# Kernel tuning notes

Measured on AMD Instinct MI355X. Metric: run time of the kernel, lower is better.

Reference implementation:

```python
import jax, jax.numpy as jnp
import numpy as np

N_OP, N_TAB, N_COL, N_PRED = 131072, 32768, 131072, 65536
NCF = 32
H = 512
NUM_GRAPHS = 64
EPS = 1e-5  # torch LayerNorm default
# fixed relation order: (src_type, dst_type)
RELS = [('table', 'operator'), ('predicate', 'operator'), ('column', 'operator'),
        ('column', 'predicate'), ('operator', 'operator'), ('table', 'table'), ('column', 'column')]
NNODE = {'operator': N_OP, 'table': N_TAB, 'column': N_COL, 'predicate': N_PRED}
EDGES = [262144, 262144, 262144, 262144, 262144, 32768, 131072]


def setup_inputs() -> dict:
    key = jax.random.key(0)
    ks = iter(jax.random.split(key, 80))
    def nrm(shape, fan_in):
        return jax.random.normal(next(ks), shape, jnp.float32) / np.sqrt(fan_in).astype(np.float32)
    inp = {
        'x_operator': jax.random.normal(next(ks), (N_OP, 4), jnp.float32),
        'x_table': jax.random.normal(next(ks), (N_TAB, 2), jnp.float32),
        'x_column': jax.random.normal(next(ks), (N_COL, NCF), jnp.float32),
        'x_predicate': jax.random.normal(next(ks), (N_PRED, 4), jnp.float32),
        'W_op': nrm((4, H), 4), 'b_op': jnp.zeros((H,), jnp.float32),
        'W_tab': nrm((2, H), 2), 'b_tab': jnp.zeros((H,), jnp.float32),
        'W_col': nrm((NCF, H), NCF), 'b_col': jnp.zeros((H,), jnp.float32),
        'W_pred': nrm((4, H), 4), 'b_pred': jnp.zeros((H,), jnp.float32),
        'conv1_Wl': nrm((7, H, H), H), 'conv1_bl': jnp.zeros((7, H), jnp.float32),
        'conv1_Wr': nrm((7, H, H), H),
        'conv2_Wl': nrm((7, H, H), H), 'conv2_bl': jnp.zeros((7, H), jnp.float32),
        'conv2_Wr': nrm((7, H, H), H),
        'g1': jnp.ones((H,), jnp.float32), 'beta1': jnp.zeros((H,), jnp.float32),
        'g2': jnp.ones((H,), jnp.float32), 'beta2': jnp.zeros((H,), jnp.float32),
        'W_out': nrm((H, 1), H), 'b_out': jnp.zeros((1,), jnp.float32),
    }
    for i, (s, d) in enumerate(RELS):
        e = EDGES[i]
        inp[f'src{i}'] = jax.random.randint(next(ks), (e,), 0, NNODE[s], jnp.int32)
        inp[f'dst{i}'] = jax.random.randint(next(ks), (e,), 0, NNODE[d], jnp.int32)
    inp['batch_operator'] = jnp.sort(jax.random.randint(next(ks), (N_OP,), 0, NUM_GRAPHS, jnp.int32))
    return inp


def _layer_norm(x, g, b):
    m = jnp.mean(x, -1, keepdims=True)
    v = jnp.mean((x - m) ** 2, -1, keepdims=True)
    return (x - m) * jax.lax.rsqrt(v + EPS) * g + b


def _segment_mean(vals, idx, n):
    s = jax.ops.segment_sum(vals, idx, num_segments=n)
    c = jax.ops.segment_sum(jnp.ones(idx.shape, vals.dtype), idx, num_segments=n)
    return s / jnp.maximum(c, 1.0)[:, None]


def _sage(x_src, x_dst, src, dst, Wl, bl, Wr, n_dst):
    # PyG SAGEConv: lin_l(mean of neighbor msgs) + lin_r(root), lin_r has no bias
    agg = _segment_mean(x_src[src], dst, n_dst)
    return agg @ Wl + bl + x_dst @ Wr


def _forward(x_operator, x_table, x_column, x_predicate,
             W_op, b_op, W_tab, b_tab, W_col, b_col, W_pred, b_pred,
             conv1_Wl, conv1_bl, conv1_Wr, conv2_Wl, conv2_bl, conv2_Wr,
             g1, beta1, g2, beta2, W_out, b_out, edges, batch_operator):
    h = {'operator': x_operator @ W_op + b_op,
         'table': x_table @ W_tab + b_tab,
         'column': x_column @ W_col + b_col,
         'predicate': x_predicate @ W_pred + b_pred}

    def hetero(h, Wl, bl, Wr):
        outs = {}
        for i, (s, d) in enumerate(RELS):
            src, dst = edges[i]
            o = _sage(h[s], h[d], src, dst, Wl[i], bl[i], Wr[i], NNODE[d])
            outs.setdefault(d, []).append(o)
        # HeteroConv aggr='mean' across relations sharing a dst node type
        return {k: sum(v) / len(v) for k, v in outs.items()}

    h = hetero(h, conv1_Wl, conv1_bl, conv1_Wr)
    h = {k: _layer_norm(jax.nn.elu(v), g1, beta1) for k, v in h.items()}  # dropout = eval identity
    h = hetero(h, conv2_Wl, conv2_bl, conv2_Wr)
    h = {k: _layer_norm(jax.nn.elu(v), g2, beta2) for k, v in h.items()}
    pooled = _segment_mean(h['operator'], batch_operator, NUM_GRAPHS)  # global_mean_pool
    return (pooled @ W_out + b_out).squeeze()


def reference(x_operator, x_table, x_column, x_predicate,
              W_op, b_op, W_tab, b_tab, W_col, b_col, W_pred, b_pred,
              conv1_Wl, conv1_bl, conv1_Wr, conv2_Wl, conv2_bl, conv2_Wr,
              g1, beta1, g2, beta2, W_out, b_out,
              src0, dst0, src1, dst1, src2, dst2, src3, dst3,
              src4, dst4, src5, dst5, src6, dst6, batch_operator):
    edges = [(src0, dst0), (src1, dst1), (src2, dst2), (src3, dst3),
             (src4, dst4), (src5, dst5), (src6, dst6)]
    return _forward(x_operator, x_table, x_column, x_predicate,
                    W_op, b_op, W_tab, b_tab, W_col, b_col, W_pred, b_pred,
                    conv1_Wl, conv1_bl, conv1_Wr, conv2_Wl, conv2_bl, conv2_Wr,
                    g1, beta1, g2, beta2, W_out, b_out, edges, batch_operator)
```

## Files before the change

kernel.cpp:

```cpp
#include <hip/hip_runtime.h>
#include <hip/hip_bf16.h>

typedef unsigned short u16;
typedef __attribute__((ext_vector_type(8))) short bf16x8;
typedef __attribute__((ext_vector_type(4))) short bf16x4;
typedef __attribute__((ext_vector_type(4))) float f32x4;

typedef __attribute__((address_space(1))) const void gv_t;
typedef __attribute__((address_space(3))) void lv_t;

#define DEVINL __device__ __forceinline__

DEVINL float bf2f(u16 s) { union { unsigned u; float f; } v; v.u = ((unsigned)s) << 16; return v.f; }
DEVINL u16 f2bf(float f) {
  union { float f; unsigned u; } v; v.f = f;
  return (u16)((v.u + 0x7FFFu + ((v.u >> 16) & 1u)) >> 16);
}

__global__ void probe_k(float* __restrict__ out, float v) { out[threadIdx.x] = v; }

struct PackPtrs { const float* wl2; const float* wr2; u16* bt[5]; };
__global__ __launch_bounds__(256) void pack_multi(PackPtrs p) {
  int j = blockIdx.x >> 10;
  int idx = (blockIdx.x & 1023) * 256 + threadIdx.x;
  int k = idx >> 9, n = idx & 511;
  float v;
  if (j < 4) {
    int r = (j == 3) ? 4 : j;
    v = p.wl2[((size_t)r * 512 + k) * 512 + n];
  } else {
    size_t o = (size_t)k * 512 + n;
    v = p.wr2[o] + p.wr2[o + 262144] + p.wr2[o + 524288] + p.wr2[o + 1048576];
  }
  p.bt[j][(size_t)n * 512 + k] = f2bf(v * 0.25f);
}

struct FoldPtrs { const float* a[8]; const float* w[2]; u16* bt[4]; };
__constant__ int   c_off[19] = {0,16,24,56,64,320,328,360,368,400,416,424,440,696,704,960,1216,1224,1256};
__constant__ int   c_ai[18]  = {0,1,2,3,4,5,6,7,6, 0,1,0, 4,5,4, 4,5,2};
__constant__ int   c_wi[18]  = {0,0,0,0,0,0,0,0,1, 0,0,1, 0,0,1, 0,0,1};
__constant__ int   c_r0[18]  = {0,0,1,1,2,2,4,4,0, 5,5,5, 6,6,6, 3,3,3};
__constant__ float c_sc[18]  = {0.25f,0.25f,0.25f,0.25f,0.25f,0.25f,0.25f,0.25f,0.25f,
                                1.f,1.f,1.f, 1.f,1.f,1.f, 1.f,1.f,1.f};
__constant__ int   c_bt[18]  = {0,0,0,0,0,0,0,0,0, 1,1,1, 2,2,2, 3,3,3};
__constant__ int   c_K[18]   = {64,64,64,64,64,64,64,64,64, 64,64,64, 128,128,128, 64,64,64};
__constant__ int   c_ko[18]  = {0,2,3,7,8,40,41,45,46, 0,2,3, 0,32,33, 0,32,33};

__global__ __launch_bounds__(256) void fold_multi(FoldPtrs p) {
  __shared__ float red[256];
  int b = blockIdx.x;
  int j = 0;
#pragma unroll
  for (int t = 1; t < 18; ++t) j += (b >= c_off[t]);
  int rel = b - c_off[j];
  int f = rel >> 3, nb = rel & 7;
  int tid = threadIdx.x;
  int n = nb * 64 + (tid & 63);
  int kg = tid >> 6;
  const float* A = p.a[c_ai[j]] + (size_t)f * 512;
  const float* W = p.w[c_wi[j]];
  int k0 = kg * 128;
  float acc = 0.f;
  if (j != 8) {
    const float* Wp = W + (size_t)c_r0[j] * 512 * 512 + n;
#pragma unroll 16
    for (int k = k0; k < k0 + 128; ++k) acc += A[k] * Wp[(size_t)k * 512];
  } else {
    const float* W0 = W + n;
    const float* W1 = W + (size_t)262144 + n;
    const float* W2 = W + (size_t)524288 + n;
    const float* W4 = W + (size_t)1048576 + n;
#pragma unroll 8
    for (int k = k0; k < k0 + 128; ++k) {
      size_t o = (size_t)k * 512;
      acc += A[k] * (W0[o] + W1[o] + W2[o] + W4[o]);
    }
  }
  red[tid] = acc;
  __syncthreads();
  if (kg == 0) {
    float v = red[tid] + red[tid + 64] + red[tid + 128] + red[tid + 192];
    p.bt[c_bt[j]][(size_t)n * c_K[j] + c_ko[j] + f] = f2bf(v * c_sc[j]);
  }
}

struct VFPtrs { const float* bl[5]; const float* bvec[5]; const float* w; float* out[5]; };
__constant__ int   c_vi[5][4] = {{0,1,2,4},{0,1,2,4},{5,-1,-1,-1},{6,-1,-1,-1},{3,-1,-1,-1}};
__constant__ float c_vs[5]    = {0.25f,0.25f,1.f,1.f,1.f};

__global__ __launch_bounds__(256) void vecfold_multi(VFPtrs p) {
  __shared__ float red[256];
  int j = blockIdx.x >> 4, blk = blockIdx.x & 15;
  int tid = threadIdx.x;
  int n = blk * 32 + (tid & 31);
  int kg = tid >> 5;
  const float* bv = p.bvec[j];
  float a = 0.f;
  if (bv) {
    int i1 = c_vi[j][1];
    const float* W0 = p.w + (size_t)c_vi[j][0] * 262144 + n;
    if (i1 < 0) {
#pragma unroll 16
      for (int k = kg * 64; k < kg * 64 + 64; ++k) a += bv[k] * W0[(size_t)k * 512];
    } else {
      const float* W1 = p.w + (size_t)c_vi[j][1] * 262144 + n;
      const float* W2 = p.w + (size_t)c_vi[j][2] * 262144 + n;
      const float* W3 = p.w + (size_t)c_vi[j][3] * 262144 + n;
#pragma unroll 8
      for (int k = kg * 64; k < kg * 64 + 64; ++k) {
        size_t o = (size_t)k * 512;
        a += bv[k] * (W0[o] + W1[o] + W2[o] + W3[o]);
      }
    }
  }
  red[tid] = a;
  __syncthreads();
  if (kg == 0) {
    float v = 0.f;
#pragma unroll
    for (int q = 0; q < 8; ++q) v += red[(tid & 31) + q * 32];
    float bsum = p.bl[j][c_vi[j][0] * 512 + n];
    if (c_vi[j][1] >= 0) {
      bsum += p.bl[j][c_vi[j][1] * 512 + n];
      bsum += p.bl[j][c_vi[j][2] * 512 + n];
      bsum += p.bl[j][c_vi[j][3] * 512 + n];
    }
    p.out[j][n] = (v + bsum) * c_vs[j];
  }
}

struct EdgePtrs { const int* dst[7]; const int* src[7]; };
__constant__ int c_hoff[8]  = {0,1024,2048,3072,4096,5120,5248,5760};
__constant__ int c_hbase[7] = {0,131072,262144,393216,458752,589824,622592};
__constant__ int c_hne[7]   = {262144,262144,262144,262144,262144,32768,131072};

__global__ __launch_bounds__(256) void hist_multi(EdgePtrs p, int* __restrict__ cnt) {
  int b = blockIdx.x;
  int j = 0;
#pragma unroll
  for (int t = 1; t < 7; ++t) j += (b >= c_hoff[t]);
  int i = (b - c_hoff[j]) * 256 + threadIdx.x;
  if (i < c_hne[j]) atomicAdd(&cnt[c_hbase[j] + p.dst[j][i]], 1);
}

__global__ __launch_bounds__(256) void fill_multi(EdgePtrs p, int* __restrict__ cursor,
                                                  int* __restrict__ esrc) {
  int b = blockIdx.x;
  int j = 0;
#pragma unroll
  for (int t = 1; t < 7; ++t) j += (b >= c_hoff[t]);
  int i = (b - c_hoff[j]) * 256 + threadIdx.x;
  if (i < c_hne[j]) {
    int pos = atomicAdd(&cursor[c_hbase[j] + p.dst[j][i]], 1);
    esrc[pos] = p.src[j][i];
  }
}

__global__ void scan1_k(const int* __restrict__ in, int* __restrict__ out,
                        int* __restrict__ part, int n) {
  __shared__ int s[256];
  int t = threadIdx.x;
  int base = blockIdx.x * 1024 + t * 4;
  int x0 = 0, x1 = 0, x2 = 0, x3 = 0;
  if (base < n) x0 = in[base];
  if (base + 1 < n) x1 = in[base + 1];
  if (base + 2 < n) x2 = in[base + 2];
  if (base + 3 < n) x3 = in[base + 3];
  int tsum = x0 + x1 + x2 + x3;
  s[t] = tsum;
  __syncthreads();
  for (int off = 1; off < 256; off <<= 1) {
    int v = (t >= off) ? s[t - off] : 0;
    __syncthreads();
    s[t] += v;
    __syncthreads();
  }
  int excl = s[t] - tsum;
  if (base < n) out[base] = excl;
  if (base + 1 < n) out[base + 1] = excl + x0;
  if (base + 2 < n) out[base + 2] = excl + x0 + x1;
  if (base + 3 < n) out[base + 3] = excl + x0 + x1 + x2;
  if (t == 255) part[blockIdx.x] = s[255];
}

__global__ void scan2_k(int* __restrict__ part, int nb) {
  __shared__ int s[1024];
  int t = threadIdx.x;
  int orig = (t < nb) ? part[t] : 0;
  s[t] = orig;
  __syncthreads();
  for (int off = 1; off < 1024; off <<= 1) {
    int v = (t >= off) ? s[t - off] : 0;
    __syncthreads();
    s[t] += v;
    __syncthreads();
  }
  if (t < nb) part[t] = s[t] - orig;
}

__global__ void scan3_k(int* __restrict__ out, int* __restrict__ cursor,
                        const int* __restrict__ part, int n) {
  int i = blockIdx.x * 256 + threadIdx.x;
  if (i < n) {
    int v = out[i] + part[i >> 10];
    out[i] = v;
    cursor[i] = v;
  }
}

__global__ void raw_agg(const int* __restrict__ offs, const int* __restrict__ esrc,
                        const float* __restrict__ x, int F, u16* __restrict__ A1,
                        int K, int colOff, int indCol, int nd) {
  int row = blockIdx.x * 32 + (threadIdx.x >> 3);
  if (row >= nd) return;
  int j = threadIdx.x & 7;
  int e0 = offs[row], e1 = offs[row + 1];
  float acc[4] = {0.f, 0.f, 0.f, 0.f};
  for (int e = e0; e < e1; ++e) {
    int s = esrc[e];
#pragma unroll
    for (int u = 0; u < 4; ++u) {
      int f = j + u * 8;
      if (f < F) acc[u] += x[(size_t)s * F + f];
    }
  }
  float inv = (e1 > e0) ? 1.f / (float)(e1 - e0) : 0.f;
#pragma unroll
  for (int u = 0; u < 4; ++u) {
    int f = j + u * 8;
    if (f < F) A1[(size_t)row * K + colOff + f] = f2bf(acc[u] * inv);
  }
  if (j == 0) A1[(size_t)row * K + indCol] = f2bf((e1 > e0) ? 1.f : 0.f);
}

struct RawPtrs { const int* offs; const int* esrc; const float* x[4]; u16* A1; };
__constant__ int c_gF[4]    = {2,4,32,4};
__constant__ int c_gco[4]   = {0,3,8,41};
__constant__ int c_gic[4]   = {2,7,40,45};
__constant__ int c_gcsrb[4] = {0,131072,262144,458752};

__global__ __launch_bounds__(256) void raw_multi(RawPtrs p, int s0) {
  int j = blockIdx.x >> 10;
  int row = (blockIdx.x & 1023) * 32 + (threadIdx.x >> 3);
  int jj = threadIdx.x & 7;
  const int* offs = p.offs + c_gcsrb[j] + s0;
  const float* x = p.x[j];
  int F = c_gF[j];
  int e0 = offs[row], e1 = offs[row + 1];
  float acc[4] = {0.f, 0.f, 0.f, 0.f};
  for (int e = e0; e < e1; ++e) {
    int s = p.esrc[e];
#pragma unroll
    for (int u = 0; u < 4; ++u) {
      int f = jj + u * 8;
      if (f < F) acc[u] += x[(size_t)s * F + f];
    }
  }
  float inv = (e1 > e0) ? 1.f / (float)(e1 - e0) : 0.f;
#pragma unroll
  for (int u = 0; u < 4; ++u) {
    int f = jj + u * 8;
    if (f < F) p.A1[(size_t)row * 64 + c_gco[j] + f] = f2bf(acc[u] * inv);
  }
  if (jj == 0) p.A1[(size_t)row * 64 + c_gic[j]] = f2bf((e1 > e0) ? 1.f : 0.f);
}

__global__ void a1_root(const float* __restrict__ x, int rowBase, u16* __restrict__ A1,
                        int K, int rootOff, int nd, int lf) {
  int idx = blockIdx.x * 256 + threadIdx.x;
  int i = idx >> lf, f = idx & ((1 << lf) - 1);
  if (i >= nd) return;
  A1[(size_t)i * K + rootOff + f] = f2bf(x[(((size_t)(rowBase + i)) << lf) + f]);
}

template <bool FIRST>
__global__ __launch_bounds__(256) void gather_acc(
    const int* __restrict__ offs, const int* __restrict__ esrc,
    const u16* __restrict__ hT, const float* __restrict__ bias,
    u16* __restrict__ acc, int s0, int s1) {
  int w = blockIdx.x * 4 + (threadIdx.x >> 6);
  int l = threadIdx.x & 63;
  int e0 = offs[w], e1 = offs[w + 1];
  float sum[8] = {0.f, 0.f, 0.f, 0.f, 0.f, 0.f, 0.f, 0.f};
  bool found = false;
  for (int e = e0; e < e1; ++e) {
    int s = esrc[e];
    if (s >= s0 && s < s1) {
      found = true;
      bf16x8 v = *(const bf16x8*)&hT[(size_t)(s - s0) * 512 + l * 8];
#pragma unroll
      for (int j = 0; j < 8; ++j) sum[j] += bf2f((u16)v[j]);
    }
  }
  float inv = (e1 > e0) ? 1.f / (float)(e1 - e0) : 0.f;
  u16* ap = acc + (size_t)w * 512 + l * 8;
  bf16x8 r;
  if (FIRST) {
#pragma unroll
    for (int j = 0; j < 8; ++j) r[j] = (short)f2bf(bias[l * 8 + j] + sum[j] * inv);
    *(bf16x8*)ap = r;
  } else {
    if (!found) return;
    bf16x8 old = *(const bf16x8*)ap;
#pragma unroll
    for (int j = 0; j < 8; ++j) r[j] = (short)f2bf(bf2f((u16)old[j]) + sum[j] * inv);
    *(bf16x8*)ap = r;
  }
}

template <bool ELU, bool ACC, int K>
__global__ __launch_bounds__(256) void gemm_k(
    const u16* __restrict__ A, const u16* __restrict__ BT,
    const float* __restrict__ bias, u16* __restrict__ C, int M) {
  __shared__ u16 As[128 * 64];
  __shared__ u16 Bs[128 * 64];
  int tid = threadIdx.x;
  int wid = tid >> 6, lane = tid & 63;
  int wm = wid >> 1, wn = wid & 1;
  int bm = blockIdx.x * 128, bn = blockIdx.y * 128;
  int r16 = lane & 15, hi4 = lane >> 4;
  int srow = tid >> 3;
  int scol = ((tid & 7) ^ (srow & 7)) * 8;
  int sw = r16 & 7;
  f32x4 acc[4][4];
#pragma unroll
  for (int i = 0; i < 4; ++i)
#pragma unroll
    for (int j = 0; j < 4; ++j) acc[i][j] = (f32x4){0.f, 0.f, 0.f, 0.f};

#pragma unroll
  for (int k0 = 0; k0 < K; k0 += 64) {
    __syncthreads();
#pragma unroll
    for (int i = 0; i < 4; ++i) {
      const u16* ga = A + (size_t)(bm + i * 32 + srow) * K + k0 + scol;
      const u16* gb = BT + (size_t)(bn + i * 32 + srow) * K + k0 + scol;
      __builtin_amdgcn_global_load_lds((gv_t*)ga, (lv_t*)(As + i * 2048 + wid * 512), 16, 0, 0);
      __builtin_amdgcn_global_load_lds((gv_t*)gb, (lv_t*)(Bs + i * 2048 + wid * 512), 16, 0, 0);
    }
    __syncthreads();
#pragma unroll
    for (int kk = 0; kk < 64; kk += 32) {
      bf16x8 af[4], bfr[4];
#pragma unroll
      for (int f = 0; f < 4; ++f) {
        int grp = (kk >> 3) + hi4;
        af[f]  = *(const bf16x8*)&As[(wm * 64 + f * 16 + r16) * 64 + ((grp ^ sw) << 3)];
        bfr[f] = *(const bf16x8*)&Bs[(wn * 64 + f * 16 + r16) * 64 + ((grp ^ sw) << 3)];
      }
#pragma unroll
      for (int mf = 0; mf < 4; ++mf)
#pragma unroll
        for (int nf = 0; nf < 4; ++nf)
          acc[mf][nf] = __builtin_amdgcn_mfma_f32_16x16x32_bf16(bfr[nf], af[mf], acc[mf][nf], 0, 0, 0);
    }
  }
#pragma unroll
  for (int mf = 0; mf < 4; ++mf) {
    int r = bm + wm * 64 + mf * 16 + r16;
#pragma unroll
    for (int nf = 0; nf < 4; ++nf) {
      int c0 = bn + wn * 64 + nf * 16 + hi4 * 4;
      u16* cp = C + (size_t)r * 512 + c0;
      bf16x4 oldv;
      if (ACC) oldv = *(const bf16x4*)cp;
      f32x4 bv;
      if (bias) bv = *(const f32x4*)&bias[c0];
      bf16x4 res;
#pragma unroll
      for (int j = 0; j < 4; ++j) {
        float v = acc[mf][nf][j] + (bias ? bv[j] : 0.f);
        if (ACC) v += bf2f((u16)oldv[j]);
        if (ELU) v = v > 0.f ? v : expm1f(v);
        res[j] = (short)f2bf(v);
      }
      *(bf16x4*)cp = res;
    }
  }
}

template <bool ACC>
__global__ __launch_bounds__(256) void gemm_t(
    const u16* __restrict__ A, const u16* __restrict__ BT, u16* __restrict__ C) {
  __shared__ u16 As[128 * 64];
  __shared__ u16 Bs[128 * 64];
  int b = blockIdx.x;
  int u = (b & 7) * 128 + (b >> 3);
  int bm = (u >> 2) * 128;
  int bn = (u & 3) * 128;
  int tid = threadIdx.x;
  int wid = tid >> 6, lane = tid & 63;
  int wm = wid >> 1, wn = wid & 1;
  int r16 = lane & 15, hi4 = lane >> 4;
  int srow = tid >> 3;
  int scol = ((tid & 7) ^ (srow & 7)) * 8;
  int sw = r16 & 7;
  f32x4 acc[4][4];
#pragma unroll
  for (int i = 0; i < 4; ++i)
#pragma unroll
    for (int j = 0; j < 4; ++j) acc[i][j] = (f32x4){0.f, 0.f, 0.f, 0.f};

#pragma unroll
  for (int k0 = 0; k0 < 512; k0 += 64) {
    __syncthreads();
#pragma unroll
    for (int i = 0; i < 4; ++i) {
      const u16* ga = A + (size_t)(bm + i * 32 + srow) * 512 + k0 + scol;
      const u16* gb = BT + (size_t)(bn + i * 32 + srow) * 512 + k0 + scol;
      __builtin_amdgcn_global_load_lds((gv_t*)ga, (lv_t*)(As + i * 2048 + wid * 512), 16, 0, 0);
      __builtin_amdgcn_global_load_lds((gv_t*)gb, (lv_t*)(Bs + i * 2048 + wid * 512), 16, 0, 0);
    }
    __syncthreads();
#pragma unroll
    for (int kk = 0; kk < 64; kk += 32) {
      bf16x8 af[4], bfr[4];
#pragma unroll
      for (int f = 0; f < 4; ++f) {
        int grp = (kk >> 3) + hi4;
        af[f]  = *(const bf16x8*)&As[(wm * 64 + f * 16 + r16) * 64 + ((grp ^ sw) << 3)];
        bfr[f] = *(const bf16x8*)&Bs[(wn * 64 + f * 16 + r16) * 64 + ((grp ^ sw) << 3)];
      }
#pragma unroll
      for (int mf = 0; mf < 4; ++mf)
#pragma unroll
        for (int nf = 0; nf < 4; ++nf)
          acc[mf][nf] = __builtin_amdgcn_mfma_f32_16x16x32_bf16(bfr[nf], af[mf], acc[mf][nf], 0, 0, 0);
    }
  }
#pragma unroll
  for (int mf = 0; mf < 4; ++mf) {
    int r = bm + wm * 64 + mf * 16 + r16;
#pragma unroll
    for (int nf = 0; nf < 4; ++nf) {
      int c0 = bn + wn * 64 + nf * 16 + hi4 * 4;
      u16* cp = C + (size_t)r * 512 + c0;
      bf16x4 res;
      if (ACC) {
        bf16x4 oldv = *(const bf16x4*)cp;
#pragma unroll
        for (int j = 0; j < 4; ++j) res[j] = (short)f2bf(acc[mf][nf][j] + bf2f((u16)oldv[j]));
      } else {
#pragma unroll
        for (int j = 0; j < 4; ++j) res[j] = (short)f2bf(acc[mf][nf][j]);
      }
      *(bf16x4*)cp = res;
    }
  }
}

__global__ void ln_rows(u16* __restrict__ H, const float* __restrict__ g,
                        const float* __restrict__ be, int rows) {
  int w = blockIdx.x * 4 + (threadIdx.x >> 6);
  if (w >= rows) return;
  int l = threadIdx.x & 63;
  u16* p = H + (size_t)w * 512 + l * 8;
  bf16x8 v = *(const bf16x8*)p;
  float x[8];
  float s = 0.f;
#pragma unroll
  for (int j = 0; j < 8; ++j) { x[j] = bf2f((u16)v[j]); s += x[j]; }
#pragma unroll
  for (int m = 1; m < 64; m <<= 1) s += __shfl_xor(s, m, 64);
  float mean = s * (1.f / 512.f);
  float q = 0.f;
#pragma unroll
  for (int j = 0; j < 8; ++j) { float d = x[j] - mean; q += d * d; }
#pragma unroll
  for (int m = 1; m < 64; m <<= 1) q += __shfl_xor(q, m, 64);
  float rsd = rsqrtf(q * (1.f / 512.f) + 1e-5f);
  bf16x8 r;
#pragma unroll
  for (int j = 0; j < 8; ++j) {
    int c = l * 8 + j;
    r[j] = (short)f2bf((x[j] - mean) * rsd * g[c] + be[c]);
  }
  *(bf16x8*)p = r;
}

DEVINL int lowb(const int* a, int n, int v) {
  int lo = 0, hi = n;
  while (lo < hi) { int m = (lo + hi) >> 1; if (a[m] < v) lo = m + 1; else hi = m; }
  return lo;
}

__global__ __launch_bounds__(256) void pool1v(const u16* __restrict__ H,
                                              const int* __restrict__ batch, int nOp,
                                              const float* __restrict__ g2,
                                              const float* __restrict__ be2,
                                              float* __restrict__ pooled,
                                              int* __restrict__ cnts) {
  __shared__ float red[4][512];
  int gr = blockIdx.x >> 4, part = blockIdx.x & 15;
  int lo = lowb(batch, nOp, gr), hi = lowb(batch, nOp, gr + 1);
  if (part == 0 && threadIdx.x == 0) cnts[gr] = hi - lo;
  int len = hi - lo;
  int chunk = (len + 15) >> 4;
  int r0 = lo + part * chunk;
  int r1 = r0 + chunk;
  if (r1 > hi) r1 = hi;
  int wv = threadIdx.x >> 6, l = threadIdx.x & 63;
  float a[8] = {0.f, 0.f, 0.f, 0.f, 0.f, 0.f, 0.f, 0.f};
  float gv[8], bv[8];
#pragma unroll
  for (int j = 0; j < 8; ++j) { gv[j] = g2[l * 8 + j]; bv[j] = be2[l * 8 + j]; }
  for (int r = r0 + wv; r < r1; r += 4) {
    bf16x8 v = *(const bf16x8*)&H[(size_t)r * 512 + l * 8];
    float x[8];
    float s = 0.f;
#pragma unroll
    for (int j = 0; j < 8; ++j) {
      x[j] = bf2f((u16)v[j]);
      x[j] = x[j] > 0.f ? x[j] : expm1f(x[j]);
      s += x[j];
    }
#pragma unroll
    for (int m = 1; m < 64; m <<= 1) s += __shfl_xor(s, m, 64);
    float mean = s * (1.f / 512.f);
    float q = 0.f;
#pragma unroll
    for (int j = 0; j < 8; ++j) { float d = x[j] - mean; q += d * d; }
#pragma unroll
    for (int m = 1; m < 64; m <<= 1) q += __shfl_xor(q, m, 64);
    float rsd = rsqrtf(q * (1.f / 512.f) + 1e-5f);
#pragma unroll
    for (int j = 0; j < 8; ++j) a[j] += (x[j] - mean) * rsd * gv[j] + bv[j];
  }
#pragma unroll
  for (int j = 0; j < 8; ++j) red[wv][l * 8 + j] = a[j];
  __syncthreads();
  if (wv == 0) {
#pragma unroll
    for (int j = 0; j < 8; ++j) {
      int c = l * 8 + j;
      float s = red[0][c] + red[1][c] + red[2][c] + red[3][c];
      atomicAdd(&pooled[gr * 512 + c], s);
    }
  }
}

__global__ void pool2(const float* __restrict__ pooled, const int* __restrict__ cnts,
                      const float* __restrict__ Wout, const float* __restrict__ bout,
                      float* __restrict__ out) {
  int gg = blockIdx.x;
  int l = threadIdx.x;
  float s = 0.f;
#pragma unroll
  for (int j = 0; j < 8; ++j) {
    int c = l * 8 + j;
    s += pooled[gg * 512 + c] * Wout[c];
  }
#pragma unroll
  for (int m = 1; m < 64; m <<= 1) s += __shfl_xor(s, m, 64);
  if (l == 0) {
    int c = cnts[gg];
    if (c < 1) c = 1;
    out[gg] = s / (float)c + bout[0];
  }
}

extern "C" void kernel_launch(void* const* d_in, const int* in_sizes, int n_in,
                              void* d_out, int out_size, void* d_ws, size_t ws_size,
                              hipStream_t stream) {
  (void)in_sizes; (void)n_in; (void)out_size;
  const float* x_op   = (const float*)d_in[0];
  const float* x_tab  = (const float*)d_in[1];
  const float* x_col  = (const float*)d_in[2];
  const float* x_pred = (const float*)d_in[3];
  const float* W_op = (const float*)d_in[4],  *b_op = (const float*)d_in[5];
  const float* W_tab = (const float*)d_in[6], *b_tab = (const float*)d_in[7];
  const float* W_col = (const float*)d_in[8], *b_col = (const float*)d_in[9];
  const float* W_pred = (const float*)d_in[10], *b_pred = (const float*)d_in[11];
  const float* Wl1 = (const float*)d_in[12];
  const float* bl1 = (const float*)d_in[13];
  const float* Wr1 = (const float*)d_in[14];
  const float* Wl2 = (const float*)d_in[15];
  const float* bl2 = (const float*)d_in[16];
  const float* Wr2 = (const float*)d_in[17];
  const float* g1  = (const float*)d_in[18];
  const float* be1 = (const float*)d_in[19];
  const float* g2  = (const float*)d_in[20];
  const float* be2 = (const float*)d_in[21];
  const float* Wout = (const float*)d_in[22];
  const float* bout = (const float*)d_in[23];
  const int* SRC[7], *DST[7];
  for (int r = 0; r < 7; ++r) { SRC[r] = (const int*)d_in[24 + 2 * r]; DST[r] = (const int*)d_in[25 + 2 * r]; }
  const int* batch = (const int*)d_in[38];
  float* out = (float*)d_out;

  const int CSRB[7] = {0, 131072, 262144, 393216, 458752, 589824, 622592};
  const int TOT = 753664;
  const int NOP = 131072;

  char* ws = (char*)d_ws;
  u16* acc     = (u16*)ws;
  u16* h1      = (u16*)(ws + 134217728ull);
  int* curFul  = (int*)(ws + 134217728ull);
  u16* hT      = (u16*)(ws + 167772160ull);
  u16* A1      = (u16*)(ws + 234881024ull);
  int* offsFul = (int*)(ws + 243269632ull);
  int* esrcFul = (int*)(ws + 246284544ull);
  u16* BT2_0   = (u16*)(ws + 252182784ull);
  u16* BT2_1   = BT2_0 + 262144;
  u16* BT2_2   = BT2_1 + 262144;
  u16* BT2_4   = BT2_2 + 262144;
  u16* BT2rt   = BT2_4 + 262144;
  u16* BT1op   = (u16*)(ws + 254804224ull);
  u16* BT1tab  = (u16*)(ws + 254869760ull);
  u16* BT1col  = (u16*)(ws + 254935296ull);
  u16* BT1pr   = (u16*)(ws + 255066368ull);
  float* b1op  = (float*)(ws + 255131904ull);
  float* b1tab = b1op + 512, *b1col = b1op + 1024, *b1pr = b1op + 1536, *b2vec = b1op + 2048;
  float* pooled = (float*)(ws + 255142144ull);
  int* cnts     = (int*)(ws + 255273216ull);
  int* part     = (int*)(ws + 255273472ull);
  const size_t WS_NEED = 255277568ull;
  if (ws_size < WS_NEED) { probe_k<<<1, 64, 0, stream>>>(out, (float)ws_size); return; }

  (void)hipMemsetAsync(curFul, 0, 3014912ull, stream);
  EdgePtrs ep;
  for (int r = 0; r < 7; ++r) { ep.dst[r] = DST[r]; ep.src[r] = SRC[r]; }
  hist_multi<<<5760, 256, 0, stream>>>(ep, curFul);
  scan1_k<<<737, 256, 0, stream>>>(curFul, offsFul, part, TOT + 1);
  scan2_k<<<1, 1024, 0, stream>>>(part, 737);
  scan3_k<<<2945, 256, 0, stream>>>(offsFul, curFul, part, TOT + 1);
  fill_multi<<<5760, 256, 0, stream>>>(ep, curFul, esrcFul);

  PackPtrs pp;
  pp.wl2 = Wl2; pp.wr2 = Wr2;
  pp.bt[0] = BT2_0; pp.bt[1] = BT2_1; pp.bt[2] = BT2_2; pp.bt[3] = BT2_4; pp.bt[4] = BT2rt;
  pack_multi<<<5120, 256, 0, stream>>>(pp);
  (void)hipMemsetAsync(BT1op, 0, 65536 + 65536 + 131072 + 65536, stream);
  FoldPtrs fp;
  fp.a[0] = W_tab; fp.a[1] = b_tab; fp.a[2] = W_pred; fp.a[3] = b_pred;
  fp.a[4] = W_col; fp.a[5] = b_col; fp.a[6] = W_op;   fp.a[7] = b_op;
  fp.w[0] = Wl1;   fp.w[1] = Wr1;
  fp.bt[0] = BT1op; fp.bt[1] = BT1tab; fp.bt[2] = BT1col; fp.bt[3] = BT1pr;
  fold_multi<<<1256, 256, 0, stream>>>(fp);
  VFPtrs vp;
  vp.bl[0] = bl2; vp.bl[1] = bl1; vp.bl[2] = bl1; vp.bl[3] = bl1; vp.bl[4] = bl1;
  vp.bvec[0] = nullptr; vp.bvec[1] = b_op; vp.bvec[2] = b_tab; vp.bvec[3] = b_col; vp.bvec[4] = b_pred;
  vp.w = Wr1;
  vp.out[0] = b2vec; vp.out[1] = b1op; vp.out[2] = b1tab; vp.out[3] = b1col; vp.out[4] = b1pr;
  vecfold_multi<<<80, 256, 0, stream>>>(vp);

  (void)hipMemsetAsync(A1, 0, 32768ull * 64 * 2, stream);
  raw_agg<<<1024, 256, 0, stream>>>(offsFul + CSRB[5], esrcFul, x_tab, 2, A1, 64, 0, 2, 32768);
  a1_root<<<256, 256, 0, stream>>>(x_tab, 0, A1, 64, 3, 32768, 1);
  gemm_k<true, false, 64><<<dim3(256, 4), 256, 0, stream>>>(A1, BT1tab, b1tab, h1, 32768);
  ln_rows<<<8192, 256, 0, stream>>>(h1, g1, be1, 32768);
  gemm_t<false><<<1024, 256, 0, stream>>>(h1, BT2_0, hT);
  gather_acc<true><<<32768, 256, 0, stream>>>(offsFul + CSRB[0], esrcFul, hT, b2vec, acc, 0, 32768);

  (void)hipMemsetAsync(A1, 0, 32768ull * 64 * 2, stream);
  for (int q = 0; q < 2; ++q) {
    int qs = q * 32768;
    raw_agg<<<1024, 256, 0, stream>>>(offsFul + CSRB[3] + qs, esrcFul, x_col, 32, A1, 64, 0, 32, 32768);
    a1_root<<<512, 256, 0, stream>>>(x_pred, qs, A1, 64, 33, 32768, 2);
    gemm_k<true, false, 64><<<dim3(256, 4), 256, 0, stream>>>(A1, BT1pr, b1pr, h1, 32768);
    ln_rows<<<8192, 256, 0, stream>>>(h1, g1, be1, 32768);
    gemm_t<false><<<1024, 256, 0, stream>>>(h1, BT2_1, hT + (size_t)qs * 512);
  }
  gather_acc<false><<<32768, 256, 0, stream>>>(offsFul + CSRB[1], esrcFul, hT, nullptr, acc, 0, 65536);

  (void)hipMemsetAsync(A1, 0, 32768ull * 128 * 2, stream);
  for (int hs = 0; hs < 2; ++hs) {
    int S0 = hs * 65536;
    for (int q = 0; q < 2; ++q) {
      int qs = S0 + q * 32768;
      raw_agg<<<1024, 256, 0, stream>>>(offsFul + CSRB[6] + qs, esrcFul, x_col, 32, A1, 128, 0, 32, 32768);
      a1_root<<<4096, 256, 0, stream>>>(x_col, qs, A1, 128, 33, 32768, 5);
      gemm_k<true, false, 128><<<dim3(256, 4), 256, 0, stream>>>(A1, BT1col, b1col, h1, 32768);
      ln_rows<<<8192, 256, 0, stream>>>(h1, g1, be1, 32768);
      gemm_t<false><<<1024, 256, 0, stream>>>(h1, BT2_2, hT + (size_t)q * 32768 * 512);
    }
    gather_acc<false><<<32768, 256, 0, stream>>>(offsFul + CSRB[2], esrcFul, hT, nullptr,
                                                 acc, S0, S0 + 65536);
  }

  (void)hipMemsetAsync(A1, 0, 32768ull * 64 * 2, stream);
  for (int hs = 0; hs < 2; ++hs) {
    int S0 = hs * 65536;
    for (int q = 0; q < 2; ++q) {
      int qs = S0 + q * 32768;
      RawPtrs rp;
      rp.offs = offsFul; rp.esrc = esrcFul; rp.A1 = A1;
      rp.x[0] = x_tab; rp.x[1] = x_pred; rp.x[2] = x_col; rp.x[3] = x_op;
      raw_multi<<<4096, 256, 0, stream>>>(rp, qs);
      a1_root<<<512, 256, 0, stream>>>(x_op, qs, A1, 64, 46, 32768, 2);
      gemm_k<true, false, 64><<<dim3(256, 4), 256, 0, stream>>>(A1, BT1op, b1op, h1, 32768);
      ln_rows<<<8192, 256, 0, stream>>>(h1, g1, be1, 32768);
      gemm_t<true><<<1024, 256, 0, stream>>>(h1, BT2rt, acc + (size_t)qs * 512);
      gemm_t<false><<<1024, 256, 0, stream>>>(h1, BT2_4, hT + (size_t)q * 32768 * 512);
    }
    gather_acc<false><<<32768, 256, 0, stream>>>(offsFul + CSRB[4], esrcFul, hT, nullptr,
                                                 acc, S0, S0 + 65536);
  }

  (void)hipMemsetAsync(pooled, 0, 64 * 512 * 4, stream);
  pool1v<<<1024, 256, 0, stream>>>(acc, batch, NOP, g2, be2, pooled, cnts);
  pool2<<<64, 64, 0, stream>>>(pooled, cnts, Wout, bout, out);
}
```

Before: 1.619 ms.

## Fold layer-1 LayerNorm into second GEMM epilogue via row stats and column sums

Replaces the in-place LayerNorm pass over h1 with a stats-only kernel that writes a per-row mean and rstd. The gamma scale is folded into the packed conv2 weights, and precomputed column sums of gamma*W and beta*W let the gemm_t epilogue apply the normalization algebraically. This removes the LN write-back of the 32768x512 activation buffer, leaving only a read. gemm_k also switches to the swizzled 1D block ordering. The change adds a small precompute kernel, and the GEMM now runs on un-normalized bf16 inputs, which may shift rounding error.

```diff
diff --git a/kernel.cpp b/kernel.cpp
--- a/kernel.cpp
+++ b/kernel.cpp
@@ -19,7 +19,7 @@
 
 __global__ void probe_k(float* __restrict__ out, float v) { out[threadIdx.x] = v; }
 
-struct PackPtrs { const float* wl2; const float* wr2; u16* bt[5]; };
+struct PackPtrs { const float* wl2; const float* wr2; const float* g1; u16* bt[5]; };
 __global__ __launch_bounds__(256) void pack_multi(PackPtrs p) {
   int j = blockIdx.x >> 10;
   int idx = (blockIdx.x & 1023) * 256 + threadIdx.x;
@@ -32,7 +32,44 @@
     size_t o = (size_t)k * 512 + n;
     v = p.wr2[o] + p.wr2[o + 262144] + p.wr2[o + 524288] + p.wr2[o + 1048576];
   }
-  p.bt[j][(size_t)n * 512 + k] = f2bf(v * 0.25f);
+  p.bt[j][(size_t)n * 512 + k] = f2bf(v * 0.25f * p.g1[k]);
+}
+
+__global__ __launch_bounds__(256) void csbb_k(const float* __restrict__ wl2,
+                                              const float* __restrict__ wr2,
+                                              const float* __restrict__ g1,
+                                              const float* __restrict__ be1,
+                                              float* __restrict__ cs, float* __restrict__ bb) {
+  __shared__ float redA[256], redB[256];
+  int j = blockIdx.x >> 4;
+  int n = (blockIdx.x & 15) * 32 + (threadIdx.x & 31);
+  int kg = threadIdx.x >> 5;
+  float a = 0.f, b = 0.f;
+  for (int k = kg * 64; k < kg * 64 + 64; ++k) {
+    float w;
+    if (j < 4) {
+      int r = (j == 3) ? 4 : j;
+      w = wl2[((size_t)r * 512 + k) * 512 + n];
+    } else {
+      size_t o = (size_t)k * 512 + n;
+      w = wr2[o] + wr2[o + 262144] + wr2[o + 524288] + wr2[o + 1048576];
+    }
+    a += g1[k] * w;
+    b += be1[k] * w;
+  }
+  redA[threadIdx.x] = a;
+  redB[threadIdx.x] = b;
+  __syncthreads();
+  if (kg == 0) {
+    float va = 0.f, vb = 0.f;
+#pragma unroll
+    for (int q = 0; q < 8; ++q) {
+      va += redA[(threadIdx.x & 31) + q * 32];
+      vb += redB[(threadIdx.x & 31) + q * 32];
+    }
+    cs[j * 512 + n] = va * 0.25f;
+    bb[j * 512 + n] = vb * 0.25f;
+  }
 }
 
 struct FoldPtrs { const float* a[8]; const float* w[2]; u16* bt[4]; };
@@ -308,80 +345,10 @@
   }
 }
 
-template <bool ELU, bool ACC, int K>
+template <bool ELU, int K>
 __global__ __launch_bounds__(256) void gemm_k(
     const u16* __restrict__ A, const u16* __restrict__ BT,
-    const float* __restrict__ bias, u16* __restrict__ C, int M) {
-  __shared__ u16 As[128 * 64];
-  __shared__ u16 Bs[128 * 64];
-  int tid = threadIdx.x;
-  int wid = tid >> 6, lane = tid & 63;
-  int wm = wid >> 1, wn = wid & 1;
-  int bm = blockIdx.x * 128, bn = blockIdx.y * 128;
-  int r16 = lane & 15, hi4 = lane >> 4;
-  int srow = tid >> 3;
-  int scol = ((tid & 7) ^ (srow & 7)) * 8;
-  int sw = r16 & 7;
-  f32x4 acc[4][4];
-#pragma unroll
-  for (int i = 0; i < 4; ++i)
-#pragma unroll
-    for (int j = 0; j < 4; ++j) acc[i][j] = (f32x4){0.f, 0.f, 0.f, 0.f};
-
-#pragma unroll
-  for (int k0 = 0; k0 < K; k0 += 64) {
-    __syncthreads();
-#pragma unroll
-    for (int i = 0; i < 4; ++i) {
-      const u16* ga = A + (size_t)(bm + i * 32 + srow) * K + k0 + scol;
-      const u16* gb = BT + (size_t)(bn + i * 32 + srow) * K + k0 + scol;
-      __builtin_amdgcn_global_load_lds((gv_t*)ga, (lv_t*)(As + i * 2048 + wid * 512), 16, 0, 0);
-      __builtin_amdgcn_global_load_lds((gv_t*)gb, (lv_t*)(Bs + i * 2048 + wid * 512), 16, 0, 0);
-    }
-    __syncthreads();
-#pragma unroll
-    for (int kk = 0; kk < 64; kk += 32) {
-      bf16x8 af[4], bfr[4];
-#pragma unroll
-      for (int f = 0; f < 4; ++f) {
-        int grp = (kk >> 3) + hi4;
-        af[f]  = *(const bf16x8*)&As[(wm * 64 + f * 16 + r16) * 64 + ((grp ^ sw) << 3)];
-        bfr[f] = *(const bf16x8*)&Bs[(wn * 64 + f * 16 + r16) * 64 + ((grp ^ sw) << 3)];
-      }
-#pragma unroll
-      for (int mf = 0; mf < 4; ++mf)
-#pragma unroll
-        for (int nf = 0; nf < 4; ++nf)
-          acc[mf][nf] = __builtin_amdgcn_mfma_f32_16x16x32_bf16(bfr[nf], af[mf], acc[mf][nf], 0, 0, 0);
-    }
-  }
-#pragma unroll
-  for (int mf = 0; mf < 4; ++mf) {
-    int r = bm + wm * 64 + mf * 16 + r16;
-#pragma unroll
-    for (int nf = 0; nf < 4; ++nf) {
-      int c0 = bn + wn * 64 + nf * 16 + hi4 * 4;
-      u16* cp = C + (size_t)r * 512 + c0;
-      bf16x4 oldv;
-      if (ACC) oldv = *(const bf16x4*)cp;
-      f32x4 bv;
-      if (bias) bv = *(const f32x4*)&bias[c0];
-      bf16x4 res;
-#pragma unroll
-      for (int j = 0; j < 4; ++j) {
-        float v = acc[mf][nf][j] + (bias ? bv[j] : 0.f);
-        if (ACC) v += bf2f((u16)oldv[j]);
-        if (ELU) v = v > 0.f ? v : expm1f(v);
-        res[j] = (short)f2bf(v);
-      }
-      *(bf16x4*)cp = res;
-    }
-  }
-}
-
-template <bool ACC>
-__global__ __launch_bounds__(256) void gemm_t(
-    const u16* __restrict__ A, const u16* __restrict__ BT, u16* __restrict__ C) {
+    const float* __restrict__ bias, u16* __restrict__ C) {
   __shared__ u16 As[128 * 64];
   __shared__ u16 Bs[128 * 64];
   int b = blockIdx.x;
@@ -402,6 +369,97 @@
     for (int j = 0; j < 4; ++j) acc[i][j] = (f32x4){0.f, 0.f, 0.f, 0.f};
 
 #pragma unroll
+  for (int k0 = 0; k0 < K; k0 += 64) {
+    __syncthreads();
+#pragma unroll
+    for (int i = 0; i < 4; ++i) {
+      const u16* ga = A + (size_t)(bm + i * 32 + srow) * K + k0 + scol;
+      const u16* gb = BT + (size_t)(bn + i * 32 + srow) * K + k0 + scol;
+      __builtin_amdgcn_global_load_lds((gv_t*)ga, (lv_t*)(As + i * 2048 + wid * 512), 16, 0, 0);
+      __builtin_amdgcn_global_load_lds((gv_t*)gb, (lv_t*)(Bs + i * 2048 + wid * 512), 16, 0, 0);
+    }
+    __syncthreads();
+#pragma unroll
+    for (int kk = 0; kk < 64; kk += 32) {
+      bf16x8 af[4], bfr[4];
+#pragma unroll
+      for (int f = 0; f < 4; ++f) {
+        int grp = (kk >> 3) + hi4;
+        af[f]  = *(const bf16x8*)&As[(wm * 64 + f * 16 + r16) * 64 + ((grp ^ sw) << 3)];
+        bfr[f] = *(const bf16x8*)&Bs[(wn * 64 + f * 16 + r16) * 64 + ((grp ^ sw) << 3)];
+      }
+#pragma unroll
+      for (int mf = 0; mf < 4; ++mf)
+#pragma unroll
+        for (int nf = 0; nf < 4; ++nf)
+          acc[mf][nf] = __builtin_amdgcn_mfma_f32_16x16x32_bf16(bfr[nf], af[mf], acc[mf][nf], 0, 0, 0);
+    }
+  }
+#pragma unroll
+  for (int mf = 0; mf < 4; ++mf) {
+    int r = bm + wm * 64 + mf * 16 + r16;
+#pragma unroll
+    for (int nf = 0; nf < 4; ++nf) {
+      int c0 = bn + wn * 64 + nf * 16 + hi4 * 4;
+      u16* cp = C + (size_t)r * 512 + c0;
+      f32x4 bv = *(const f32x4*)&bias[c0];
+      bf16x4 res;
+#pragma unroll
+      for (int j = 0; j < 4; ++j) {
+        float v = acc[mf][nf][j] + bv[j];
+        if (ELU) v = v > 0.f ? v : expm1f(v);
+        res[j] = (short)f2bf(v);
+      }
+      *(bf16x4*)cp = res;
+    }
+  }
+}
+
+__global__ void ln_stats(const u16* __restrict__ H, float2* __restrict__ stats, int rows) {
+  int w = blockIdx.x * 4 + (threadIdx.x >> 6);
+  if (w >= rows) return;
+  int l = threadIdx.x & 63;
+  bf16x8 v = *(const bf16x8*)&H[(size_t)w * 512 + l * 8];
+  float x[8];
+  float s = 0.f;
+#pragma unroll
+  for (int j = 0; j < 8; ++j) { x[j] = bf2f((u16)v[j]); s += x[j]; }
+#pragma unroll
+  for (int m = 1; m < 64; m <<= 1) s += __shfl_xor(s, m, 64);
+  float mean = s * (1.f / 512.f);
+  float q = 0.f;
+#pragma unroll
+  for (int j = 0; j < 8; ++j) { float d = x[j] - mean; q += d * d; }
+#pragma unroll
+  for (int m = 1; m < 64; m <<= 1) q += __shfl_xor(q, m, 64);
+  if (l == 0) stats[w] = make_float2(mean, rsqrtf(q * (1.f / 512.f) + 1e-5f));
+}
+
+template <bool ACC>
+__global__ __launch_bounds__(256) void gemm_t(
+    const u16* __restrict__ A, const u16* __restrict__ BT, u16* __restrict__ C,
+    const float2* __restrict__ stats, const float* __restrict__ cs,
+    const float* __restrict__ bb) {
+  __shared__ u16 As[128 * 64];
+  __shared__ u16 Bs[128 * 64];
+  int b = blockIdx.x;
+  int u = (b & 7) * 128 + (b >> 3);
+  int bm = (u >> 2) * 128;
+  int bn = (u & 3) * 128;
+  int tid = threadIdx.x;
+  int wid = tid >> 6, lane = tid & 63;
+  int wm = wid >> 1, wn = wid & 1;
+  int r16 = lane & 15, hi4 = lane >> 4;
+  int srow = tid >> 3;
+  int scol = ((tid & 7) ^ (srow & 7)) * 8;
+  int sw = r16 & 7;
+  f32x4 acc[4][4];
+#pragma unroll
+  for (int i = 0; i < 4; ++i)
+#pragma unroll
+    for (int j = 0; j < 4; ++j) acc[i][j] = (f32x4){0.f, 0.f, 0.f, 0.f};
+
+#pragma unroll
   for (int k0 = 0; k0 < 512; k0 += 64) {
     __syncthreads();
 #pragma unroll
@@ -431,51 +489,32 @@
 #pragma unroll
   for (int mf = 0; mf < 4; ++mf) {
     int r = bm + wm * 64 + mf * 16 + r16;
+    float2 st = stats[r];
+    float mr = st.x * st.y;
 #pragma unroll
     for (int nf = 0; nf < 4; ++nf) {
       int c0 = bn + wn * 64 + nf * 16 + hi4 * 4;
       u16* cp = C + (size_t)r * 512 + c0;
+      f32x4 csv = *(const f32x4*)&cs[c0];
+      f32x4 bbv = *(const f32x4*)&bb[c0];
       bf16x4 res;
       if (ACC) {
         bf16x4 oldv = *(const bf16x4*)cp;
 #pragma unroll
-        for (int j = 0; j < 4; ++j) res[j] = (short)f2bf(acc[mf][nf][j] + bf2f((u16)oldv[j]));
+        for (int j = 0; j < 4; ++j) {
+          float v = st.y * acc[mf][nf][j] - mr * csv[j] + bbv[j] + bf2f((u16)oldv[j]);
+          res[j] = (short)f2bf(v);
+        }
       } else {
 #pragma unroll
-        for (int j = 0; j < 4; ++j) res[j] = (short)f2bf(acc[mf][nf][j]);
+        for (int j = 0; j < 4; ++j) {
+          float v = st.y * acc[mf][nf][j] - mr * csv[j] + bbv[j];
+          res[j] = (short)f2bf(v);
+        }
       }
       *(bf16x4*)cp = res;
     }
   }
-}
-
-__global__ void ln_rows(u16* __restrict__ H, const float* __restrict__ g,
-                        const float* __restrict__ be, int rows) {
-  int w = blockIdx.x * 4 + (threadIdx.x >> 6);
-  if (w >= rows) return;
-  int l = threadIdx.x & 63;
-  u16* p = H + (size_t)w * 512 + l * 8;
-  bf16x8 v = *(const bf16x8*)p;
-  float x[8];
-  float s = 0.f;
-#pragma unroll
-  for (int j = 0; j < 8; ++j) { x[j] = bf2f((u16)v[j]); s += x[j]; }
-#pragma unroll
-  for (int m = 1; m < 64; m <<= 1) s += __shfl_xor(s, m, 64);
-  float mean = s * (1.f / 512.f);
-  float q = 0.f;
-#pragma unroll
-  for (int j = 0; j < 8; ++j) { float d = x[j] - mean; q += d * d; }
-#pragma unroll
-  for (int m = 1; m < 64; m <<= 1) q += __shfl_xor(q, m, 64);
-  float rsd = rsqrtf(q * (1.f / 512.f) + 1e-5f);
-  bf16x8 r;
-#pragma unroll
-  for (int j = 0; j < 8; ++j) {
-    int c = l * 8 + j;
-    r[j] = (short)f2bf((x[j] - mean) * rsd * g[c] + be[c]);
-  }
-  *(bf16x8*)p = r;
 }
 
 DEVINL int lowb(const int* a, int n, int v) {
@@ -614,7 +653,10 @@
   float* pooled = (float*)(ws + 255142144ull);
   int* cnts     = (int*)(ws + 255273216ull);
   int* part     = (int*)(ws + 255273472ull);
-  const size_t WS_NEED = 255277568ull;
+  float2* stats = (float2*)(ws + 255277568ull);
+  float* cs     = (float*)(ws + 255539712ull);
+  float* bb     = (float*)(ws + 255549952ull);
+  const size_t WS_NEED = 255560192ull;
   if (ws_size < WS_NEED) { probe_k<<<1, 64, 0, stream>>>(out, (float)ws_size); return; }
 
   (void)hipMemsetAsync(curFul, 0, 3014912ull, stream);
@@ -627,9 +669,10 @@
   fill_multi<<<5760, 256, 0, stream>>>(ep, curFul, esrcFul);
 
   PackPtrs pp;
-  pp.wl2 = Wl2; pp.wr2 = Wr2;
+  pp.wl2 = Wl2; pp.wr2 = Wr2; pp.g1 = g1;
   pp.bt[0] = BT2_0; pp.bt[1] = BT2_1; pp.bt[2] = BT2_2; pp.bt[3] = BT2_4; pp.bt[4] = BT2rt;
   pack_multi<<<5120, 256, 0, stream>>>(pp);
+  csbb_k<<<80, 256, 0, stream>>>(Wl2, Wr2, g1, be1, cs, bb);
   (void)hipMemsetAsync(BT1op, 0, 65536 + 65536 + 131072 + 65536, stream);
   FoldPtrs fp;
   fp.a[0] = W_tab; fp.a[1] = b_tab; fp.a[2] = W_pred; fp.a[3] = b_pred;
@@ -644,12 +687,15 @@
   vp.out[0] = b2vec; vp.out[1] = b1op; vp.out[2] = b1tab; vp.out[3] = b1col; vp.out[4] = b1pr;
   vecfold_multi<<<80, 256, 0, stream>>>(vp);
 
+  float* cs0 = cs, *cs1 = cs + 512, *cs2 = cs + 1024, *cs4 = cs + 1536, *csrt = cs + 2048;
+  float* bb0 = bb, *bb1 = bb + 512, *bb2 = bb + 1024, *bb4 = bb + 1536, *bbrt = bb + 2048;
+
   (void)hipMemsetAsync(A1, 0, 32768ull * 64 * 2, stream);
   raw_agg<<<1024, 256, 0, stream>>>(offsFul + CSRB[5], esrcFul, x_tab, 2, A1, 64, 0, 2, 32768);
   a1_root<<<256, 256, 0, stream>>>(x_tab, 0, A1, 64, 3, 32768, 1);
-  gemm_k<true, false, 64><<<dim3(256, 4), 256, 0, stream>>>(A1, BT1tab, b1tab, h1, 32768);
-  ln_rows<<<8192, 256, 0, stream>>>(h1, g1, be1, 32768);
-  gemm_t<false><<<1024, 256, 0, stream>>>(h1, BT2_0, hT);
+  gemm_k<true, 64><<<1024, 256, 0, stream>>>(A1, BT1tab, b1tab, h1);
+  ln_stats<<<8192, 256, 0, stream>>>(h1, stats, 32768);
+  gemm_t<false><<<1024, 256, 0, stream>>>(h1, BT2_0, hT, stats, cs0, bb0);
   gather_acc<true><<<32768, 256, 0, stream>>>(offsFul + CSRB[0], esrcFul, hT, b2vec, acc, 0, 32768);
 
   (void)hipMemsetAsync(A1, 0, 32768ull * 64 * 2, stream);
@@ -657,9 +703,9 @@
     int qs = q * 32768;
     raw_agg<<<1024, 256, 0, stream>>>(offsFul + CSRB[3] + qs, esrcFul, x_col, 32, A1, 64, 0, 32, 32768);
     a1_root<<<512, 256, 0, stream>>>(x_pred, qs, A1, 64, 33, 32768, 2);
-    gemm_k<true, false, 64><<<dim3(256, 4), 256, 0, stream>>>(A1, BT1pr, b1pr, h1, 32768);
-    ln_rows<<<8192, 256, 0, stream>>>(h1, g1, be1, 32768);
-    gemm_t<false><<<1024, 256, 0, stream>>>(h1, BT2_1, hT + (size_t)qs * 512);
+    gemm_k<true, 64><<<1024, 256, 0, stream>>>(A1, BT1pr, b1pr, h1);
+    ln_stats<<<8192, 256, 0, stream>>>(h1, stats, 32768);
+    gemm_t<false><<<1024, 256, 0, stream>>>(h1, BT2_1, hT + (size_t)qs * 512, stats, cs1, bb1);
   }
   gather_acc<false><<<32768, 256, 0, stream>>>(offsFul + CSRB[1], esrcFul, hT, nullptr, acc, 0, 65536);
 
@@ -670,9 +716,9 @@
       int qs = S0 + q * 32768;
       raw_agg<<<1024, 256, 0, stream>>>(offsFul + CSRB[6] + qs, esrcFul, x_col, 32, A1, 128, 0, 32, 32768);
       a1_root<<<4096, 256, 0, stream>>>(x_col, qs, A1, 128, 33, 32768, 5);
-      gemm_k<true, false, 128><<<dim3(256, 4), 256, 0, stream>>>(A1, BT1col, b1col, h1, 32768);
-      ln_rows<<<8192, 256, 0, stream>>>(h1, g1, be1, 32768);
-      gemm_t<false><<<1024, 256, 0, stream>>>(h1, BT2_2, hT + (size_t)q * 32768 * 512);
+      gemm_k<true, 128><<<1024, 256, 0, stream>>>(A1, BT1col, b1col, h1);
+      ln_stats<<<8192, 256, 0, stream>>>(h1, stats, 32768);
+      gemm_t<false><<<1024, 256, 0, stream>>>(h1, BT2_2, hT + (size_t)q * 32768 * 512, stats, cs2, bb2);
     }
     gather_acc<false><<<32768, 256, 0, stream>>>(offsFul + CSRB[2], esrcFul, hT, nullptr,
                                                  acc, S0, S0 + 65536);
@@ -688,10 +734,10 @@
       rp.x[0] = x_tab; rp.x[1] = x_pred; rp.x[2] = x_col; rp.x[3] = x_op;
       raw_multi<<<4096, 256, 0, stream>>>(rp, qs);
       a1_root<<<512, 256, 0, stream>>>(x_op, qs, A1, 64, 46, 32768, 2);
-      gemm_k<true, false, 64><<<dim3(256, 4), 256, 0, stream>>>(A1, BT1op, b1op, h1, 32768);
-      ln_rows<<<8192, 256, 0, stream>>>(h1, g1, be1, 32768);
-      gemm_t<true><<<1024, 256, 0, stream>>>(h1, BT2rt, acc + (size_t)qs * 512);
-      gemm_t<false><<<1024, 256, 0, stream>>>(h1, BT2_4, hT + (size_t)q * 32768 * 512);
+      gemm_k<true, 64><<<1024, 256, 0, stream>>>(A1, BT1op, b1op, h1);
+      ln_stats<<<8192, 256, 0, stream>>>(h1, stats, 32768);
+      gemm_t<true><<<1024, 256, 0, stream>>>(h1, BT2rt, acc + (size_t)qs * 512, stats, csrt, bbrt);
+      gemm_t<false><<<1024, 256, 0, stream>>>(h1, BT2_4, hT + (size_t)q * 32768 * 512, stats, cs4, bb4);
     }
     gather_acc<false><<<32768, 256, 0, stream>>>(offsFul + CSRB[4], esrcFul, hT, nullptr,
                                                  acc, S0, S0 + 65536);
```

New measurement: 1.614 ms. No clear change (-0.3%).
